# Kernel optimization log

Measured on AMD Instinct MI355X. Metric: run time of the kernel, lower is better.

The kernel has to match this reference:

```python
import jax, jax.numpy as jnp
import numpy as np

N_NODES = 50000
N_EDGES = 1600000
IN_C, HID_C, OUT_C = 1433, 128, 47


def setup_inputs() -> dict:
    key = jax.random.key(0)
    ks = jax.random.split(key, 5)
    x = jax.random.normal(ks[0], (N_NODES, IN_C), dtype=jnp.float32)
    edge_index = jax.random.randint(ks[1], (2, N_EDGES), 0, N_NODES, dtype=jnp.int32)
    # Glorot-ish init scaled by fan-in
    W1 = jax.random.normal(ks[2], (IN_C, HID_C), dtype=jnp.float32) / np.sqrt(IN_C)
    W2 = jax.random.normal(ks[3], (HID_C, HID_C), dtype=jnp.float32) / np.sqrt(HID_C)
    W3 = jax.random.normal(ks[4], (HID_C, OUT_C), dtype=jnp.float32) / np.sqrt(HID_C)
    b1 = jnp.zeros((HID_C,), jnp.float32)
    b2 = jnp.zeros((HID_C,), jnp.float32)
    b3 = jnp.zeros((OUT_C,), jnp.float32)
    return {"x": x, "edge_index": edge_index, "W1": W1, "b1": b1,
            "W2": W2, "b2": b2, "W3": W3, "b3": b3}


def _gcn_norm(edge_index, n_nodes, dtype):
    # PyG GCNConv default: add self-loops, symmetric D^-1/2 A D^-1/2 norm.
    loops = jnp.arange(n_nodes, dtype=edge_index.dtype)
    src = jnp.concatenate([edge_index[0], loops])
    dst = jnp.concatenate([edge_index[1], loops])
    deg = jax.ops.segment_sum(jnp.ones(src.shape[0], dtype), dst, num_segments=n_nodes)
    dinv = jax.lax.rsqrt(jnp.maximum(deg, 1.0))  # deg >= 1 due to self-loops
    norm = dinv[src] * dinv[dst]  # [E + N]
    return src, dst, norm


def _gcn_layer(h, W, b, src, dst, norm, n_nodes):
    hw = h @ W                       # [N, C_out] dense transform first (cheaper)
    msg = hw[src] * norm[:, None]    # gather + per-edge scale
    out = jax.ops.segment_sum(msg, dst, num_segments=n_nodes)  # scatter-add
    return out + b


def reference(x, edge_index, W1, b1, W2, b2, W3, b3):
    n = x.shape[0]
    src, dst, norm = _gcn_norm(edge_index, n, x.dtype)
    h = jax.nn.relu(_gcn_layer(x, W1, b1, src, dst, norm, n))
    # dropout is identity in eval mode (training=False)
    h = jax.nn.relu(_gcn_layer(h, W2, b2, src, dst, norm, n))
    return _gcn_layer(h, W3, b3, src, dst, norm, n)
```

## Files before the change

### kernel.cpp

```cpp
#include <hip/hip_runtime.h>
#include <math.h>
#include <stdint.h>

#define N_NODES 50000
#define N_EDGES 1600000
#define IN_C    1433
#define HID_C   128
#define OUT_C   47
#define KPAD1   1440

typedef unsigned short u16;

__device__ inline u16 f2bf(float x, float& hf) {
    unsigned u = __float_as_uint(x);
    unsigned r = (u + 0x7FFFu + ((u >> 16) & 1u)) & 0xFFFF0000u;
    hf = __uint_as_float(r);
    return (u16)(r >> 16);
}

__device__ inline void gld_lds16(const void* g, const void* lds) {
    __builtin_amdgcn_global_load_lds(
        (const __attribute__((address_space(1))) unsigned int*)(unsigned long long)(uintptr_t)g,
        (__attribute__((address_space(3))) unsigned int*)(unsigned long long)(unsigned)(uintptr_t)lds,
        16, 0, 0);
}

__device__ inline void wg_barrier() {
    asm volatile("" ::: "memory");
    __builtin_amdgcn_s_barrier();
    asm volatile("" ::: "memory");
}

__global__ __launch_bounds__(256) void k_zero_i(int* p, int n) {
    int i = blockIdx.x * 256 + threadIdx.x;
    if (i < n) p[i] = 0;
}

__global__ __launch_bounds__(256) void k_count(const int* __restrict__ dst, int* __restrict__ cnt) {
    int e = blockIdx.x * 256 + threadIdx.x;
    if (e < N_EDGES) atomicAdd(&cnt[dst[e]], 1);
}

__global__ __launch_bounds__(256) void k_dinv(const int* __restrict__ cnt, float* __restrict__ dinv) {
    int i = blockIdx.x * 256 + threadIdx.x;
    if (i < N_NODES) dinv[i] = rsqrtf(1.0f + (float)cnt[i]);
}

__global__ __launch_bounds__(1024) void k_scan(const int* __restrict__ cnt, int* __restrict__ row_start) {
    __shared__ int sums[1024];
    const int t = threadIdx.x;
    const int CH = (N_NODES + 1023) / 1024;
    const int base = t * CH;
    int s = 0;
    for (int j = 0; j < CH; ++j) { int idx = base + j; if (idx < N_NODES) s += cnt[idx]; }
    sums[t] = s;
    __syncthreads();
    for (int off = 1; off < 1024; off <<= 1) {
        int v = (t >= off) ? sums[t - off] : 0;
        __syncthreads();
        sums[t] += v;
        __syncthreads();
    }
    int run = (t == 0) ? 0 : sums[t - 1];
    for (int j = 0; j < CH; ++j) {
        int idx = base + j;
        if (idx < N_NODES) { row_start[idx] = run; run += cnt[idx]; }
    }
    if (t == 1023) row_start[N_NODES] = N_EDGES;
}

__global__ __launch_bounds__(256) void k_fill(
    const int* __restrict__ src, const int* __restrict__ dst,
    const int* __restrict__ row_start, int* __restrict__ cursor,
    int* __restrict__ csr_src)
{
    int e = blockIdx.x * 256 + threadIdx.x;
    if (e >= N_EDGES) return;
    int t = dst[e];
    int pos = row_start[t] + atomicAdd(&cursor[t], 1);
    csr_src[pos] = src[e];
}

__global__ __launch_bounds__(256) void k_wsplit(
    const float* __restrict__ W, int K, int Kpad,
    u16* __restrict__ Thi, u16* __restrict__ Tlo)
{
    int id = blockIdx.x * 256 + threadIdx.x;
    if (id >= 128 * Kpad) return;
    int n = id / Kpad, k = id - n * Kpad;
    float v = (k < K) ? W[(long)k * HID_C + n] : 0.f;
    float hf; u16 h = f2bf(v, hf);
    float d;  u16 l = f2bf(v - hf, d);
    Thi[id] = h; Tlo[id] = l;
}

template<bool RELU_A>
__global__ __launch_bounds__(256) void k_gemm_mfma(
    const float* __restrict__ A, const u16* __restrict__ BThi,
    const u16* __restrict__ BTlo, float* __restrict__ C,
    int M, int K, int Kpad, int lda)
{
    using bf16x8 = __attribute__((ext_vector_type(8))) short;
    using f32x4  = __attribute__((ext_vector_type(4))) float;

    __shared__ float Af[2][2048];
    __shared__ u16  Bhs[2][4096];
    __shared__ u16  Bls[2][4096];

    const int tid  = threadIdx.x;
    const int wave = tid >> 6, lane = tid & 63;
    const int lr   = lane & 15, quad = lane >> 4;
    const int wm   = (wave >> 1) * 32, wn = (wave & 1) * 64;
    const int m0   = blockIdx.x * 64;

    f32x4 acc[2][4];
#pragma unroll
    for (int i = 0; i < 2; ++i)
#pragma unroll
        for (int j = 0; j < 4; ++j)
#pragma unroll
            for (int r = 0; r < 4; ++r) acc[i][j][r] = 0.f;

    const int nk = (K + 31) >> 5;

    auto stageB = [&](int t, int buf) {
        const int k0 = t * 32;
#pragma unroll
        for (int i = 0; i < 2; ++i) {
            const int gc  = wave * 128 + i * 64;
            const int g   = gc + lane;
            const int row = g >> 2, c = g & 3;
            const int q   = c ^ ((row >> 1) & 3);
            const long goff = (long)row * Kpad + k0 + q * 8;
            gld_lds16(BThi + goff, &Bhs[buf][gc * 8]);
            gld_lds16(BTlo + goff, &Bls[buf][gc * 8]);
        }
    };
    auto stageA = [&](int t, int buf) {
        const int k0 = t * 32;
        if (k0 + 32 <= K) {
#pragma unroll
            for (int i = 0; i < 2; ++i) {
                const int gc  = wave * 128 + i * 64;
                const int g   = gc + lane;
                const int row = g >> 3, c = g & 7;
                const int q   = c ^ (row & 7);
                int gm = m0 + row; if (gm >= M) gm = M - 1;
                gld_lds16(A + (long)gm * lda + k0 + q * 4, &Af[buf][gc * 4]);
            }
        } else {
#pragma unroll
            for (int i = 0; i < 2; ++i) {
                const int g   = wave * 128 + i * 64 + lane;
                const int row = g >> 3, c = g & 7;
                const int q   = c ^ (row & 7);
                int gm = m0 + row; if (gm >= M) gm = M - 1;
                const float* p = A + (long)gm * lda;
                const int kb = k0 + q * 4;
                float4 v;
                v.x = (kb + 0 < K) ? p[kb + 0] : 0.f;
                v.y = (kb + 1 < K) ? p[kb + 1] : 0.f;
                v.z = (kb + 2 < K) ? p[kb + 2] : 0.f;
                v.w = (kb + 3 < K) ? p[kb + 3] : 0.f;
                *(float4*)&Af[buf][g * 4] = v;
            }
            asm volatile("s_waitcnt lgkmcnt(0)" ::: "memory");
        }
    };

    stageA(0, 0); stageB(0, 0);

    for (int t = 0; t < nk; ++t) {
        const int buf = t & 1;
        if (t + 1 < nk) {
            stageA(t + 1, buf ^ 1);
            stageB(t + 1, buf ^ 1);
            asm volatile("s_waitcnt vmcnt(6)" ::: "memory");
        } else {
            asm volatile("s_waitcnt vmcnt(0)" ::: "memory");
        }
        wg_barrier();

        bf16x8 ah[2], al[2];
#pragma unroll
        for (int i = 0; i < 2; ++i) {
            const int row = wm + i * 16 + lr;
            const int rx  = row & 7;
            f32x4 x0 = *(const f32x4*)&Af[buf][row * 32 + (((2 * quad)     ^ rx) * 4)];
            f32x4 x1 = *(const f32x4*)&Af[buf][row * 32 + (((2 * quad + 1) ^ rx) * 4)];
            float a8[8] = {x0[0], x0[1], x0[2], x0[3], x1[0], x1[1], x1[2], x1[3]};
#pragma unroll
            for (int c = 0; c < 8; ++c) {
                float x = RELU_A ? fmaxf(a8[c], 0.f) : a8[c];
                float hf; u16 h = f2bf(x, hf);
                float d;  u16 l = f2bf(x - hf, d);
                ah[i][c] = (short)h; al[i][c] = (short)l;
            }
        }
        bf16x8 bh[4], bl[4];
#pragma unroll
        for (int j = 0; j < 4; ++j) {
            const int row = wn + j * 16 + lr;
            const int cs  = quad ^ ((row >> 1) & 3);
            bh[j] = *(const bf16x8*)&Bhs[buf][row * 32 + cs * 8];
            bl[j] = *(const bf16x8*)&Bls[buf][row * 32 + cs * 8];
        }
#pragma unroll
        for (int i = 0; i < 2; ++i)
#pragma unroll
            for (int j = 0; j < 4; ++j) {
                acc[i][j] = __builtin_amdgcn_mfma_f32_16x16x32_bf16(ah[i], bh[j], acc[i][j], 0, 0, 0);
                acc[i][j] = __builtin_amdgcn_mfma_f32_16x16x32_bf16(ah[i], bl[j], acc[i][j], 0, 0, 0);
                acc[i][j] = __builtin_amdgcn_mfma_f32_16x16x32_bf16(al[i], bh[j], acc[i][j], 0, 0, 0);
            }
        wg_barrier();
    }

#pragma unroll
    for (int i = 0; i < 2; ++i)
#pragma unroll
        for (int r = 0; r < 4; ++r) {
            int row = m0 + wm + i * 16 + quad * 4 + r;
            if (row < M) {
#pragma unroll
                for (int j = 0; j < 4; ++j)
                    C[(long)row * HID_C + wn + j * 16 + lr] = acc[i][j][r];
            }
        }
}

template<int BN, bool RELU_A, bool BIAS>
__global__ __launch_bounds__(256) void k_gemm(
    const float* __restrict__ A, const float* __restrict__ B,
    const float* __restrict__ bias, float* __restrict__ C,
    int M, int N, int K, int lda, int ldb, int ldc)
{
    constexpr int BM = 64, BK = 16;
    constexpr int TNV = BN / 64;
    __shared__ float As[BK][BM + 4];
    __shared__ float Bs[BK][BN];

    const int tid = threadIdx.x;
    const int tm = tid >> 4;
    const int tn = tid & 15;
    const int m0 = blockIdx.x * BM;
    const int n0 = blockIdx.y * BN;

    float acc[4][TNV * 4];
#pragma unroll
    for (int r = 0; r < 4; ++r)
#pragma unroll
        for (int c = 0; c < TNV * 4; ++c) acc[r][c] = 0.f;

    for (int k0 = 0; k0 < K; k0 += BK) {
        {
            int kk = tid & 15;
            int r0 = tid >> 4;
#pragma unroll
            for (int it = 0; it < 4; ++it) {
                int r = r0 + 16 * it;
                int gm = m0 + r, gk = k0 + kk;
                float v = 0.f;
                if (gm < M && gk < K) v = A[(long)gm * lda + gk];
                if (RELU_A) v = fmaxf(v, 0.f);
                As[kk][r] = v;
            }
        }
        {
            constexpr int KPP = 256 / BN;
            int n  = tid % BN;
            int kb = tid / BN;
#pragma unroll
            for (int it = 0; it < BK / KPP; ++it) {
                int kk = kb + KPP * it;
                int gk = k0 + kk, gn = n0 + n;
                float v = 0.f;
                if (gk < K && gn < N) v = B[(long)gk * ldb + gn];
                Bs[kk][n] = v;
            }
        }
        __syncthreads();
#pragma unroll
        for (int kk = 0; kk < BK; ++kk) {
            float4 a = *(const float4*)&As[kk][tm * 4];
            float av[4] = {a.x, a.y, a.z, a.w};
#pragma unroll
            for (int j = 0; j < TNV; ++j) {
                float4 b = *(const float4*)&Bs[kk][tn * 4 + 64 * j];
                float bv[4] = {b.x, b.y, b.z, b.w};
#pragma unroll
                for (int r = 0; r < 4; ++r)
#pragma unroll
                    for (int c = 0; c < 4; ++c)
                        acc[r][c + j * 4] += av[r] * bv[c];
            }
        }
        __syncthreads();
    }
#pragma unroll
    for (int r = 0; r < 4; ++r) {
        int gm = m0 + tm * 4 + r;
        if (gm >= M) continue;
#pragma unroll
        for (int j = 0; j < TNV; ++j)
#pragma unroll
            for (int c = 0; c < 4; ++c) {
                int gn = n0 + tn * 4 + 64 * j + c;
                if (gn < N) {
                    float v = acc[r][c + j * 4];
                    if (BIAS) v += bias[gn];
                    C[(long)gm * ldc + gn] = v;
                }
            }
    }
}

template<bool RELU_IN, bool BIAS>
__global__ __launch_bounds__(256) void k_aggregate(
    const float2* __restrict__ hw, const int* __restrict__ row_start,
    const int* __restrict__ csr_src, const float* __restrict__ dinv,
    const float* __restrict__ bias, float2* __restrict__ out)
{
    const int tid = threadIdx.x;
    const int node = blockIdx.x * 4 + (tid >> 6);
    if (node >= N_NODES) return;
    const int lane = tid & 63;

    float dt = dinv[node];
    float2 v = hw[(long)node * 64 + lane];
    if (RELU_IN) { v.x = fmaxf(v.x, 0.f); v.y = fmaxf(v.y, 0.f); }
    float2 acc = {0.f, 0.f};

    const int e1 = row_start[node + 1];
    int e = row_start[node];
    for (; e + 8 <= e1; e += 8) {
        int s[8];
#pragma unroll
        for (int q = 0; q < 8; ++q) s[q] = csr_src[e + q];
        float w[8];
#pragma unroll
        for (int q = 0; q < 8; ++q) w[q] = dinv[s[q]];
        float2 u[8];
#pragma unroll
        for (int q = 0; q < 8; ++q) u[q] = hw[(long)s[q] * 64 + lane];
#pragma unroll
        for (int q = 0; q < 8; ++q) {
            if (RELU_IN) { u[q].x = fmaxf(u[q].x, 0.f); u[q].y = fmaxf(u[q].y, 0.f); }
            acc.x += w[q] * u[q].x;
            acc.y += w[q] * u[q].y;
        }
    }
    for (; e + 4 <= e1; e += 4) {
        int s0 = csr_src[e],     s1 = csr_src[e + 1];
        int s2 = csr_src[e + 2], s3 = csr_src[e + 3];
        float w0 = dinv[s0], w1 = dinv[s1], w2 = dinv[s2], w3 = dinv[s3];
        float2 u0 = hw[(long)s0 * 64 + lane];
        float2 u1 = hw[(long)s1 * 64 + lane];
        float2 u2 = hw[(long)s2 * 64 + lane];
        float2 u3 = hw[(long)s3 * 64 + lane];
        if (RELU_IN) {
            u0.x = fmaxf(u0.x, 0.f); u0.y = fmaxf(u0.y, 0.f);
            u1.x = fmaxf(u1.x, 0.f); u1.y = fmaxf(u1.y, 0.f);
            u2.x = fmaxf(u2.x, 0.f); u2.y = fmaxf(u2.y, 0.f);
            u3.x = fmaxf(u3.x, 0.f); u3.y = fmaxf(u3.y, 0.f);
        }
        acc.x += w0 * u0.x + w1 * u1.x + w2 * u2.x + w3 * u3.x;
        acc.y += w0 * u0.y + w1 * u1.y + w2 * u2.y + w3 * u3.y;
    }
    for (; e + 2 <= e1; e += 2) {
        int s0 = csr_src[e], s1 = csr_src[e + 1];
        float w0 = dinv[s0], w1 = dinv[s1];
        float2 u0 = hw[(long)s0 * 64 + lane];
        float2 u1 = hw[(long)s1 * 64 + lane];
        if (RELU_IN) {
            u0.x = fmaxf(u0.x, 0.f); u0.y = fmaxf(u0.y, 0.f);
            u1.x = fmaxf(u1.x, 0.f); u1.y = fmaxf(u1.y, 0.f);
        }
        acc.x += w0 * u0.x + w1 * u1.x;
        acc.y += w0 * u0.y + w1 * u1.y;
    }
    if (e < e1) {
        int s0 = csr_src[e];
        float w0 = dinv[s0];
        float2 u0 = hw[(long)s0 * 64 + lane];
        if (RELU_IN) { u0.x = fmaxf(u0.x, 0.f); u0.y = fmaxf(u0.y, 0.f); }
        acc.x += w0 * u0.x;
        acc.y += w0 * u0.y;
    }

    float2 r;
    r.x = dt * (acc.x + dt * v.x);
    r.y = dt * (acc.y + dt * v.y);
    if (BIAS) {
        float2 b = ((const float2*)bias)[lane];
        r.x += b.x; r.y += b.y;
    }
    out[(long)node * 64 + lane] = r;
}

__global__ __launch_bounds__(256) void k_aggregate47(
    const float* __restrict__ hw, const int* __restrict__ row_start,
    const int* __restrict__ csr_src, const float* __restrict__ dinv,
    const float* __restrict__ bias, float* __restrict__ out)
{
    const int tid = threadIdx.x;
    const int node = blockIdx.x * 4 + (tid >> 6);
    if (node >= N_NODES) return;
    const int lane = tid & 63;
    if (lane >= OUT_C) return;

    float dt = dinv[node];
    float v = hw[(long)node * 48 + lane];
    float acc = 0.f;

    const int e1 = row_start[node + 1];
    int e = row_start[node];
    for (; e + 4 <= e1; e += 4) {
        int s0 = csr_src[e],     s1 = csr_src[e + 1];
        int s2 = csr_src[e + 2], s3 = csr_src[e + 3];
        float w0 = dinv[s0], w1 = dinv[s1], w2 = dinv[s2], w3 = dinv[s3];
        float u0 = hw[(long)s0 * 48 + lane];
        float u1 = hw[(long)s1 * 48 + lane];
        float u2 = hw[(long)s2 * 48 + lane];
        float u3 = hw[(long)s3 * 48 + lane];
        acc += w0 * u0 + w1 * u1 + w2 * u2 + w3 * u3;
    }
    for (; e + 2 <= e1; e += 2) {
        int s0 = csr_src[e], s1 = csr_src[e + 1];
        float w0 = dinv[s0], w1 = dinv[s1];
        float u0 = hw[(long)s0 * 48 + lane];
        float u1 = hw[(long)s1 * 48 + lane];
        acc += w0 * u0 + w1 * u1;
    }
    if (e < e1) {
        int s0 = csr_src[e];
        acc += dinv[s0] * hw[(long)s0 * 48 + lane];
    }

    out[(long)node * OUT_C + lane] = dt * (acc + dt * v) + bias[lane];
}

extern "C" void kernel_launch(void* const* d_in, const int* in_sizes, int n_in,
                              void* d_out, int out_size, void* d_ws, size_t ws_size,
                              hipStream_t stream) {
    const float* x  = (const float*)d_in[0];
    const int*   ei = (const int*)  d_in[1];
    const float* W1 = (const float*)d_in[2];
    const float* b1 = (const float*)d_in[3];
    const float* W2 = (const float*)d_in[4];
    const float* b2 = (const float*)d_in[5];
    const float* W3 = (const float*)d_in[6];
    const float* b3 = (const float*)d_in[7];
    float* out = (float*)d_out;
    const int* src = ei;
    const int* dst = ei + N_EDGES;

    char* ws = (char*)d_ws;
    float* dinv      = (float*)(ws + 0);
    int*   cnt       = (int*)  (ws + 200192);
    int*   cursor    = (int*)  (ws + 400384);
    int*   row_start = (int*)  (ws + 600576);
    int*   csr_src   = (int*)  (ws + 801280);
    float* bufA      = (float*)(ws + 7201280);
    float* bufB      = (float*)(ws + 32801280);
    u16*   W1Thi     = (u16*)  (ws + 58401280);
    u16*   W1Tlo     = (u16*)  (ws + 58769920);
    u16*   W2Thi     = (u16*)  (ws + 59138560);
    u16*   W2Tlo     = (u16*)  (ws + 59171328);

    dim3 blk(256);
    const int gN  = (N_NODES + 255) / 256;
    const int gE  = (N_EDGES + 255) / 256;
    const int gAg = (N_NODES + 3) / 4;
    const int gMf = (N_NODES + 63) / 64;
    dim3 gGemm((N_NODES + 63) / 64, 1);

    k_zero_i<<<gN, blk, 0, stream>>>(cnt, N_NODES);
    k_zero_i<<<gN, blk, 0, stream>>>(cursor, N_NODES);
    k_count<<<gE, blk, 0, stream>>>(dst, cnt);
    k_dinv<<<gN, blk, 0, stream>>>(cnt, dinv);
    k_scan<<<1, 1024, 0, stream>>>(cnt, row_start);
    k_fill<<<gE, blk, 0, stream>>>(src, dst, row_start, cursor, csr_src);

    k_wsplit<<<(128 * KPAD1 + 255) / 256, blk, 0, stream>>>(W1, IN_C, KPAD1, W1Thi, W1Tlo);
    k_wsplit<<<(128 * HID_C + 255) / 256, blk, 0, stream>>>(W2, HID_C, HID_C, W2Thi, W2Tlo);

    k_gemm_mfma<false><<<gMf, blk, 0, stream>>>(x, W1Thi, W1Tlo, bufA, N_NODES, IN_C, KPAD1, IN_C);
    k_aggregate<false, true><<<gAg, blk, 0, stream>>>(
        (const float2*)bufA, row_start, csr_src, dinv, b1, (float2*)bufB);

    k_gemm_mfma<true><<<gMf, blk, 0, stream>>>(bufB, W2Thi, W2Tlo, bufA, N_NODES, HID_C, HID_C, HID_C);
    k_aggregate<false, true><<<gAg, blk, 0, stream>>>(
        (const float2*)bufA, row_start, csr_src, dinv, b2, (float2*)bufB);

    k_gemm<64, true, false><<<gGemm, blk, 0, stream>>>(
        bufB, W3, nullptr, bufA, N_NODES, OUT_C, HID_C, HID_C, OUT_C, 48);
    k_aggregate47<<<gAg, blk, 0, stream>>>(
        bufA, row_start, csr_src, dinv, b3, out);
}
```

Measured before the change: 691.9 us.

## Enlarge MFMA GEMM tile to 128 rows with 512 threads and merge setup kernels

The split-bf16 MFMA GEMM now uses 512-thread blocks covering 128 rows, so each staged B tile (hi/lo weights) is reused by twice as many rows. Each wave stages half as much B, and the vmcnt wait is adjusted to match. Separately, the two zeroing kernels and the two weight-split kernels are merged, and dinv is folded into the scan kernel, which cuts the number of launches. The larger tile doubles LDS use for A and halves the grid, which may lower occupancy and tail parallelism.

```diff
diff --git a/kernel.cpp b/kernel.cpp
--- a/kernel.cpp
+++ b/kernel.cpp
@@ -31,9 +31,9 @@
     asm volatile("" ::: "memory");
 }
 
-__global__ __launch_bounds__(256) void k_zero_i(int* p, int n) {
+__global__ __launch_bounds__(256) void k_zero2(int* a, int* b, int n) {
     int i = blockIdx.x * 256 + threadIdx.x;
-    if (i < n) p[i] = 0;
+    if (i < n) { a[i] = 0; b[i] = 0; }
 }
 
 __global__ __launch_bounds__(256) void k_count(const int* __restrict__ dst, int* __restrict__ cnt) {
@@ -41,12 +41,9 @@
     if (e < N_EDGES) atomicAdd(&cnt[dst[e]], 1);
 }
 
-__global__ __launch_bounds__(256) void k_dinv(const int* __restrict__ cnt, float* __restrict__ dinv) {
-    int i = blockIdx.x * 256 + threadIdx.x;
-    if (i < N_NODES) dinv[i] = rsqrtf(1.0f + (float)cnt[i]);
-}
-
-__global__ __launch_bounds__(1024) void k_scan(const int* __restrict__ cnt, int* __restrict__ row_start) {
+__global__ __launch_bounds__(1024) void k_scan(const int* __restrict__ cnt,
+                                               int* __restrict__ row_start,
+                                               float* __restrict__ dinv) {
     __shared__ int sums[1024];
     const int t = threadIdx.x;
     const int CH = (N_NODES + 1023) / 1024;
@@ -64,7 +61,11 @@
     int run = (t == 0) ? 0 : sums[t - 1];
     for (int j = 0; j < CH; ++j) {
         int idx = base + j;
-        if (idx < N_NODES) { row_start[idx] = run; run += cnt[idx]; }
+        if (idx < N_NODES) {
+            int cv = cnt[idx];
+            row_start[idx] = run; run += cv;
+            dinv[idx] = rsqrtf(1.0f + (float)cv);
+        }
     }
     if (t == 1023) row_start[N_NODES] = N_EDGES;
 }
@@ -81,21 +82,32 @@
     csr_src[pos] = src[e];
 }
 
-__global__ __launch_bounds__(256) void k_wsplit(
-    const float* __restrict__ W, int K, int Kpad,
-    u16* __restrict__ Thi, u16* __restrict__ Tlo)
+__global__ __launch_bounds__(256) void k_wsplit2(
+    const float* __restrict__ W1, const float* __restrict__ W2,
+    u16* __restrict__ T1h, u16* __restrict__ T1l,
+    u16* __restrict__ T2h, u16* __restrict__ T2l)
 {
     int id = blockIdx.x * 256 + threadIdx.x;
-    if (id >= 128 * Kpad) return;
-    int n = id / Kpad, k = id - n * Kpad;
-    float v = (k < K) ? W[(long)k * HID_C + n] : 0.f;
-    float hf; u16 h = f2bf(v, hf);
-    float d;  u16 l = f2bf(v - hf, d);
-    Thi[id] = h; Tlo[id] = l;
+    const int n1 = 128 * KPAD1;
+    if (id < n1) {
+        int n = id / KPAD1, k = id - n * KPAD1;
+        float v = (k < IN_C) ? W1[(long)k * HID_C + n] : 0.f;
+        float hf; u16 h = f2bf(v, hf);
+        float d;  u16 l = f2bf(v - hf, d);
+        T1h[id] = h; T1l[id] = l;
+    } else {
+        id -= n1;
+        if (id >= 128 * HID_C) return;
+        int n = id / HID_C, k = id - n * HID_C;
+        float v = W2[(long)k * HID_C + n];
+        float hf; u16 h = f2bf(v, hf);
+        float d;  u16 l = f2bf(v - hf, d);
+        T2h[id] = h; T2l[id] = l;
+    }
 }
 
 template<bool RELU_A>
-__global__ __launch_bounds__(256) void k_gemm_mfma(
+__global__ __launch_bounds__(512) void k_gemm_mfma(
     const float* __restrict__ A, const u16* __restrict__ BThi,
     const u16* __restrict__ BTlo, float* __restrict__ C,
     int M, int K, int Kpad, int lda)
@@ -103,7 +115,7 @@
     using bf16x8 = __attribute__((ext_vector_type(8))) short;
     using f32x4  = __attribute__((ext_vector_type(4))) float;
 
-    __shared__ float Af[2][2048];
+    __shared__ float Af[2][4096];
     __shared__ u16  Bhs[2][4096];
     __shared__ u16  Bls[2][4096];
 
@@ -111,7 +123,7 @@
     const int wave = tid >> 6, lane = tid & 63;
     const int lr   = lane & 15, quad = lane >> 4;
     const int wm   = (wave >> 1) * 32, wn = (wave & 1) * 64;
-    const int m0   = blockIdx.x * 64;
+    const int m0   = blockIdx.x * 128;
 
     f32x4 acc[2][4];
 #pragma unroll
@@ -125,16 +137,13 @@
 
     auto stageB = [&](int t, int buf) {
         const int k0 = t * 32;
-#pragma unroll
-        for (int i = 0; i < 2; ++i) {
-            const int gc  = wave * 128 + i * 64;
-            const int g   = gc + lane;
-            const int row = g >> 2, c = g & 3;
-            const int q   = c ^ ((row >> 1) & 3);
-            const long goff = (long)row * Kpad + k0 + q * 8;
-            gld_lds16(BThi + goff, &Bhs[buf][gc * 8]);
-            gld_lds16(BTlo + goff, &Bls[buf][gc * 8]);
-        }
+        const int gc  = wave * 64;
+        const int g   = gc + lane;
+        const int row = g >> 2, c = g & 3;
+        const int q   = c ^ ((row >> 1) & 3);
+        const long goff = (long)row * Kpad + k0 + q * 8;
+        gld_lds16(BThi + goff, &Bhs[buf][gc * 8]);
+        gld_lds16(BTlo + goff, &Bls[buf][gc * 8]);
     };
     auto stageA = [&](int t, int buf) {
         const int k0 = t * 32;
@@ -175,7 +184,7 @@
         if (t + 1 < nk) {
             stageA(t + 1, buf ^ 1);
             stageB(t + 1, buf ^ 1);
-            asm volatile("s_waitcnt vmcnt(6)" ::: "memory");
+            asm volatile("s_waitcnt vmcnt(4)" ::: "memory");
         } else {
             asm volatile("s_waitcnt vmcnt(0)" ::: "memory");
         }
@@ -472,24 +481,22 @@
     const int gN  = (N_NODES + 255) / 256;
     const int gE  = (N_EDGES + 255) / 256;
     const int gAg = (N_NODES + 3) / 4;
-    const int gMf = (N_NODES + 63) / 64;
+    const int gMf = (N_NODES + 127) / 128;
+    const int gWs = (128 * (KPAD1 + HID_C) + 255) / 256;
     dim3 gGemm((N_NODES + 63) / 64, 1);
 
-    k_zero_i<<<gN, blk, 0, stream>>>(cnt, N_NODES);
-    k_zero_i<<<gN, blk, 0, stream>>>(cursor, N_NODES);
+    k_zero2<<<gN, blk, 0, stream>>>(cnt, cursor, N_NODES);
     k_count<<<gE, blk, 0, stream>>>(dst, cnt);
-    k_dinv<<<gN, blk, 0, stream>>>(cnt, dinv);
-    k_scan<<<1, 1024, 0, stream>>>(cnt, row_start);
+    k_scan<<<1, 1024, 0, stream>>>(cnt, row_start, dinv);
     k_fill<<<gE, blk, 0, stream>>>(src, dst, row_start, cursor, csr_src);
 
-    k_wsplit<<<(128 * KPAD1 + 255) / 256, blk, 0, stream>>>(W1, IN_C, KPAD1, W1Thi, W1Tlo);
-    k_wsplit<<<(128 * HID_C + 255) / 256, blk, 0, stream>>>(W2, HID_C, HID_C, W2Thi, W2Tlo);
-
-    k_gemm_mfma<false><<<gMf, blk, 0, stream>>>(x, W1Thi, W1Tlo, bufA, N_NODES, IN_C, KPAD1, IN_C);
+    k_wsplit2<<<gWs, blk, 0, stream>>>(W1, W2, W1Thi, W1Tlo, W2Thi, W2Tlo);
+
+    k_gemm_mfma<false><<<gMf, dim3(512), 0, stream>>>(x, W1Thi, W1Tlo, bufA, N_NODES, IN_C, KPAD1, IN_C);
     k_aggregate<false, true><<<gAg, blk, 0, stream>>>(
         (const float2*)bufA, row_start, csr_src, dinv, b1, (float2*)bufB);
 
-    k_gemm_mfma<true><<<gMf, blk, 0, stream>>>(bufB, W2Thi, W2Tlo, bufA, N_NODES, HID_C, HID_C, HID_C);
+    k_gemm_mfma<true><<<gMf, dim3(512), 0, stream>>>(bufB, W2Thi, W2Tlo, bufA, N_NODES, HID_C, HID_C, HID_C);
     k_aggregate<false, true><<<gAg, blk, 0, stream>>>(
         (const float2*)bufA, row_start, csr_src, dinv, b2, (float2*)bufB);
 
```

Measured after the change: 713.9 us. +3.2%, slower.
